# Kernel tuning notes

Hardware: AMD Instinct MI355X
Metric: run time of the kernel (lower is better)

## Reference

```python
import jax, jax.numpy as jnp
import numpy as np
from jax import lax

B, CR, CS = 2, 256, 512
HR = WR = 64
HS = WS = 32
D_INNER, D_STATE, DT_RANK, D_CONV = 512, 16, 16, 3
EPS = 1e-5


def setup_inputs() -> dict:
    key = jax.random.key(0)
    ks = jax.random.split(key, 16)
    s = 0.02
    return {
        "resnet_feat": jax.random.normal(ks[0], (B, CR, HR, WR), jnp.float32),
        "scp_feat": jax.random.normal(ks[1], (B, CS, HS, WS), jnp.float32),
        "scp_proj_w": jax.random.normal(ks[2], (CR, CS), jnp.float32) * s,
        "scp_bn_g": jnp.ones((CR,), jnp.float32),
        "scp_bn_b": jnp.zeros((CR,), jnp.float32),
        "scp_bn_m": jax.random.normal(ks[3], (CR,), jnp.float32) * 0.1,
        "scp_bn_v": jax.random.uniform(ks[4], (CR,), jnp.float32, minval=0.5, maxval=1.5),
        "res_bn_g": jnp.ones((CR,), jnp.float32),
        "res_bn_b": jnp.zeros((CR,), jnp.float32),
        "res_bn_m": jax.random.normal(ks[5], (CR,), jnp.float32) * 0.1,
        "res_bn_v": jax.random.uniform(ks[6], (CR,), jnp.float32, minval=0.5, maxval=1.5),
        "ln_g": jnp.ones((CR,), jnp.float32),
        "ln_b": jnp.zeros((CR,), jnp.float32),
        "in_proj_w": jax.random.normal(ks[7], (2 * D_INNER, CR), jnp.float32) * s,
        "conv_w": jax.random.normal(ks[8], (D_INNER, 1, D_CONV), jnp.float32) * s,
        "conv_b": jnp.zeros((D_INNER,), jnp.float32),
        "x_proj_w": jax.random.normal(ks[9], (DT_RANK + 2 * D_STATE, D_INNER), jnp.float32) * s,
        "dt_proj_w": jax.random.normal(ks[10], (D_INNER, DT_RANK), jnp.float32) * s,
        "dt_proj_b": jnp.full((D_INNER,), -4.6, jnp.float32),  # softplus -> dt ~ 0.01
        "A_log": jnp.log(jnp.broadcast_to(jnp.arange(1, D_STATE + 1, dtype=jnp.float32), (D_INNER, D_STATE))),
        "D": jnp.ones((D_INNER,), jnp.float32),
        "out_proj_w": jax.random.normal(ks[11], (CR, D_INNER), jnp.float32) * s,
    }


def _bn(x, g, b, m, v):
    # eval-mode BatchNorm2d with running stats, NCHW
    inv = g / jnp.sqrt(v + EPS)
    return x * inv[None, :, None, None] + (b - m * inv)[None, :, None, None]


def reference(resnet_feat, scp_feat, scp_proj_w, scp_bn_g, scp_bn_b, scp_bn_m, scp_bn_v,
              res_bn_g, res_bn_b, res_bn_m, res_bn_v, ln_g, ln_b, in_proj_w, conv_w, conv_b,
              x_proj_w, dt_proj_w, dt_proj_b, A_log, D, out_proj_w):
    # --- fusion prelude ---
    rn = _bn(resnet_feat, res_bn_g, res_bn_b, res_bn_m, res_bn_v)
    sp = jnp.einsum('bchw,oc->bohw', scp_feat, scp_proj_w)        # 1x1 conv, no bias
    sp = _bn(sp, scp_bn_g, scp_bn_b, scp_bn_m, scp_bn_v)
    sp = jax.image.resize(sp, (B, CR, HR, WR), method='bilinear')  # align_corners=False semantics
    fused = rn + sp                                               # (B, CR, HR, WR)

    # --- Mamba2DBlock ---
    L = HR * WR
    x_seq = fused.transpose(0, 2, 3, 1).reshape(B, L, CR)
    mu = x_seq.mean(-1, keepdims=True)
    var = x_seq.var(-1, keepdims=True)
    xn = (x_seq - mu) / jnp.sqrt(var + EPS) * ln_g + ln_b         # LayerNorm

    xz = xn @ in_proj_w.T                                         # (B, L, 2*d_inner)
    xm, z = jnp.split(xz, 2, axis=-1)

    # causal depthwise conv1d over sequence
    xc = xm.transpose(0, 2, 1)                                    # (B, d_inner, L)
    xc = jnp.pad(xc, ((0, 0), (0, 0), (D_CONV - 1, 0)))
    xc = lax.conv_general_dilated(xc, conv_w, (1,), 'VALID',
                                  dimension_numbers=('NCH', 'OIH', 'NCH'),
                                  feature_group_count=D_INNER) + conv_b[None, :, None]
    u = jax.nn.silu(xc.transpose(0, 2, 1))                        # (B, L, d_inner)

    x_dbl = u @ x_proj_w.T                                        # (B, L, dt_rank + 2*d_state)
    dt_in, Bc, Cc = jnp.split(x_dbl, [DT_RANK, DT_RANK + D_STATE], axis=-1)
    dt = jax.nn.softplus(dt_in @ dt_proj_w.T + dt_proj_b)         # (B, L, d_inner)

    A = -jnp.exp(A_log)                                           # (d_inner, d_state)
    dA = jnp.exp(dt[..., None] * A)                               # (B, L, d_inner, d_state)
    dBu = dt[..., None] * Bc[:, :, None, :] * u[..., None]        # (B, L, d_inner, d_state)

    def comb(c1, c2):
        a1, b1 = c1
        a2, b2 = c2
        return a1 * a2, a2 * b1 + b2

    _, h = lax.associative_scan(comb, (dA, dBu), axis=1)          # h: (B, L, d_inner, d_state)
    y = jnp.einsum('blds,bls->bld', h, Cc) + u * D
    y = y * jax.nn.silu(z)
    out_seq = y @ out_proj_w.T                                    # (B, L, CR)
    out = out_seq.reshape(B, HR, WR, CR).transpose(0, 3, 1, 2)
    return fused + out
```

## Files before the change

### kernel.cpp

```cpp
#include <hip/hip_runtime.h>
#include <hip/hip_bf16.h>
#include <math.h>

typedef unsigned short u16;
typedef __attribute__((ext_vector_type(8))) short short8;
typedef __attribute__((ext_vector_type(4))) float f32x4;
typedef __attribute__((ext_vector_type(4))) unsigned short u16x4;

#define DEVINL static __device__ __forceinline__

DEVINL float b2f(u16 x) {
    union { unsigned u; float f; } v; v.u = ((unsigned)x) << 16; return v.f;
}
DEVINL u16 f2b(float f) {
    union { unsigned u; float f; } v; v.f = f;
    unsigned u = v.u;
    return (u16)((u + 0x7fffu + ((u >> 16) & 1u)) >> 16);
}
DEVINL float silu(float x) { return x / (1.f + __expf(-x)); }
DEVINL float ld_any(bool f32, const void* p, size_t i) {
    return f32 ? ((const float*)p)[i] : b2f(((const u16*)p)[i]);
}
template<bool F32> DEVINL float LDs(const void* p, size_t i) {
    if constexpr (F32) return ((const float*)p)[i];
    else               return b2f(((const u16*)p)[i]);
}

#define O_INW  0
#define O_XPW  262144
#define O_OPW  286720
#define O_SPW  417792
#define O_CW   548864
#define O_CB   550400
#define O_DTW  550912
#define O_ALOG 559104
#define O_DTB  567296
#define O_DW   567808
#define O_SG   568320
#define O_SB   568576
#define O_SM   568832
#define O_SV   569088
#define O_RG   569344
#define O_RB   569600
#define O_RM   569856
#define O_RV   570112
#define O_LG   570368
#define O_LB   570624
#define N_CVT  570880

__global__ __launch_bounds__(1024) void k_detect(const u16* __restrict__ raw,
                                                 int* __restrict__ flag)
{
    int tid = threadIdx.x;
    int cnt = 0;
    for (int i = tid; i < 131072; i += 1024) {
        float v = b2f(raw[i]);
        if (!(fabsf(v) <= 1e3f)) cnt++;
    }
#pragma unroll
    for (int off = 1; off < 64; off <<= 1) cnt += __shfl_xor(cnt, off);
    __shared__ int s16[16];
    if ((tid & 63) == 0) s16[tid >> 6] = cnt;
    __syncthreads();
    if (tid == 0) {
        int c = 0;
#pragma unroll
        for (int w = 0; w < 16; ++w) c += s16[w];
        flag[0] = (c > 0) ? 1 : 0;
    }
}

DEVINL void tr_tile(bool f32, const void* src, u16* dst, int R, int C,
                    int c0, int r0, int b, int tid)
{
    __shared__ u16 t[64][66];
    int lane = tid & 63, grp = tid >> 6;
#pragma unroll
    for (int j = 0; j < 16; ++j) {
        int rl = j * 4 + grp;
        t[rl][lane] = f2b(ld_any(f32, src, ((size_t)b * R + r0 + rl) * C + c0 + lane));
    }
    __syncthreads();
#pragma unroll
    for (int j = 0; j < 16; ++j) {
        int cl = j * 4 + grp;
        dst[((size_t)b * C + c0 + cl) * R + r0 + lane] = t[lane][cl];
    }
}

__global__ __launch_bounds__(256) void k_prep(const int* __restrict__ flag,
    const void* inw, const void* xpw, const void* opw, const void* spw,
    const void* cw, const void* cb, const void* dtw, const void* alog,
    const void* dtb, const void* Dw,
    const void* sg, const void* sb, const void* sm, const void* sv,
    const void* rg, const void* rb, const void* rm, const void* rv,
    const void* lg, const void* lb,
    const void* scp, const void* resnet,
    u16* __restrict__ w16, u16* __restrict__ scpT, u16* __restrict__ resnetT)
{
    bool f32 = (*flag != 0);
    int bid = blockIdx.x, tid = threadIdx.x;
    if (bid < 2230) {
        int i = bid * 256 + tid;
        const void* src; int off = i;
        if      (i < O_XPW)  { src = inw; }
        else if (i < O_OPW)  { src = xpw;  off = i - O_XPW; }
        else if (i < O_SPW)  { src = opw;  off = i - O_OPW; }
        else if (i < O_CW)   { src = spw;  off = i - O_SPW; }
        else if (i < O_CB)   { src = cw;   off = i - O_CW; }
        else if (i < O_DTW)  { src = cb;   off = i - O_CB; }
        else if (i < O_ALOG) { src = dtw;  off = i - O_DTW; }
        else if (i < O_DTB)  { src = alog; off = i - O_ALOG; }
        else if (i < O_DW)   { src = dtb;  off = i - O_DTB; }
        else if (i < O_SG)   { src = Dw;   off = i - O_DW; }
        else if (i < O_SB)   { src = sg;   off = i - O_SG; }
        else if (i < O_SM)   { src = sb;   off = i - O_SB; }
        else if (i < O_SV)   { src = sm;   off = i - O_SM; }
        else if (i < O_RG)   { src = sv;   off = i - O_SV; }
        else if (i < O_RB)   { src = rg;   off = i - O_RG; }
        else if (i < O_RM)   { src = rb;   off = i - O_RB; }
        else if (i < O_RV)   { src = rm;   off = i - O_RM; }
        else if (i < O_LG)   { src = rv;   off = i - O_RV; }
        else if (i < O_LB)   { src = lg;   off = i - O_LG; }
        else                 { src = lb;   off = i - O_LB; }
        w16[i] = f2b(ld_any(f32, src, off));
    } else if (bid < 2230 + 256) {
        int t = bid - 2230;
        tr_tile(f32, scp, scpT, 512, 1024, (t & 15) * 64, ((t >> 4) & 7) * 64, t >> 7, tid);
    } else {
        int t = bid - 2486;
        tr_tile(f32, resnet, resnetT, 256, 4096, (t & 63) * 64, ((t >> 6) & 3) * 64, t >> 8, tid);
    }
}

__global__ __launch_bounds__(256) void k_scpmm(
    const u16* __restrict__ scpT, const u16* __restrict__ w16,
    u16* __restrict__ sp16)
{
    const int N = 256, K = 512;
    int tid = threadIdx.x, lane = tid & 63, wid = tid >> 6;
    int ln = lane & 15, q = lane >> 4;
    int m0 = blockIdx.x * 64 + (wid & 1) * 32;
    int n0 = blockIdx.y * 64 + (wid >> 1) * 32;
    f32x4 acc00 = {0.f,0.f,0.f,0.f}, acc01 = acc00, acc10 = acc00, acc11 = acc00;
    const u16* Ap0 = scpT + (size_t)(m0 + ln) * K + q * 8;
    const u16* Ap1 = Ap0 + (size_t)16 * K;
    const u16* Wp = w16 + O_SPW;
#pragma unroll 4
    for (int k0 = 0; k0 < K; k0 += 32) {
        int kk = k0 + q * 8;
        short8 a0 = *reinterpret_cast<const short8*>(Ap0 + k0);
        short8 a1 = *reinterpret_cast<const short8*>(Ap1 + k0);
        short8 b0 = *reinterpret_cast<const short8*>(Wp + (size_t)(n0 + ln) * K + kk);
        short8 b1 = *reinterpret_cast<const short8*>(Wp + (size_t)(n0 + ln + 16) * K + kk);
        acc00 = __builtin_amdgcn_mfma_f32_16x16x32_bf16(a0, b0, acc00, 0, 0, 0);
        acc01 = __builtin_amdgcn_mfma_f32_16x16x32_bf16(a0, b1, acc01, 0, 0, 0);
        acc10 = __builtin_amdgcn_mfma_f32_16x16x32_bf16(a1, b0, acc10, 0, 0, 0);
        acc11 = __builtin_amdgcn_mfma_f32_16x16x32_bf16(a1, b1, acc11, 0, 0, 0);
    }
    int r0 = m0 + q * 4, c0 = n0 + ln;
    float inv0 = b2f(w16[O_SG + c0]) * rsqrtf(b2f(w16[O_SV + c0]) + 1e-5f);
    float sh0  = b2f(w16[O_SB + c0]) - b2f(w16[O_SM + c0]) * inv0;
    float inv1 = b2f(w16[O_SG + c0 + 16]) * rsqrtf(b2f(w16[O_SV + c0 + 16]) + 1e-5f);
    float sh1  = b2f(w16[O_SB + c0 + 16]) - b2f(w16[O_SM + c0 + 16]) * inv1;
#pragma unroll
    for (int r = 0; r < 4; ++r) {
        sp16[(size_t)(r0 + r) * N + c0]           = f2b(acc00[r] * inv0 + sh0);
        sp16[(size_t)(r0 + r) * N + c0 + 16]      = f2b(acc01[r] * inv1 + sh1);
        sp16[(size_t)(r0 + 16 + r) * N + c0]      = f2b(acc10[r] * inv0 + sh0);
        sp16[(size_t)(r0 + 16 + r) * N + c0 + 16] = f2b(acc11[r] * inv1 + sh1);
    }
}

__global__ __launch_bounds__(256) void k_ln(
    const u16* __restrict__ resnetT, const u16* __restrict__ w16,
    const u16* __restrict__ sp16, u16* __restrict__ xn)
{
    __shared__ float red[8];
    int c = threadIdx.x, b = blockIdx.y;
    float inv = b2f(w16[O_RG + c]) * rsqrtf(b2f(w16[O_RV + c]) + 1e-5f);
    float sh  = b2f(w16[O_RB + c]) - b2f(w16[O_RM + c]) * inv;
    float lgv = b2f(w16[O_LG + c]), lbv = b2f(w16[O_LB + c]);
    const u16* spc = sp16 + (size_t)b * 1024 * 256 + c;
    for (int j = 0; j < 8; ++j) {
        int l = blockIdx.x * 8 + j;
        int h = l >> 6, w = l & 63;
        float rr = b2f(resnetT[((size_t)b * 4096 + l) * 256 + c]);
        float rn = rr * inv + sh;
        float xh = 0.5f * h - 0.25f; int jh = (int)floorf(xh); float fh = xh - jh;
        float xw = 0.5f * w - 0.25f; int jw = (int)floorf(xw); float fw = xw - jw;
        int h0 = jh < 0 ? 0 : jh, h1 = jh + 1 > 31 ? 31 : jh + 1;
        int w0 = jw < 0 ? 0 : jw, w1 = jw + 1 > 31 ? 31 : jw + 1;
        float v00 = b2f(spc[(size_t)(h0 * 32 + w0) * 256]), v01 = b2f(spc[(size_t)(h0 * 32 + w1) * 256]);
        float v10 = b2f(spc[(size_t)(h1 * 32 + w0) * 256]), v11 = b2f(spc[(size_t)(h1 * 32 + w1) * 256]);
        float sp = (1.f - fh) * ((1.f - fw) * v00 + fw * v01)
                 + fh * ((1.f - fw) * v10 + fw * v11);
        float fv = rn + sp;

        float s = fv, s2 = fv * fv;
#pragma unroll
        for (int off = 1; off < 64; off <<= 1) {
            s  += __shfl_xor(s, off);
            s2 += __shfl_xor(s2, off);
        }
        int wv = c >> 6;
        if ((c & 63) == 0) { red[wv] = s; red[4 + wv] = s2; }
        __syncthreads();
        float S  = red[0] + red[1] + red[2] + red[3];
        float S2 = red[4] + red[5] + red[6] + red[7];
        __syncthreads();
        float mu   = S * (1.f / 256.f);
        float var  = S2 * (1.f / 256.f) - mu * mu;
        float rstd = rsqrtf(var + 1e-5f);
        xn[((size_t)b * 4096 + l) * 256 + c] = f2b((fv - mu) * rstd * lgv + lbv);
    }
}

__global__ __launch_bounds__(256) void k_gemm_in(
    const u16* __restrict__ A, const u16* __restrict__ w16, u16* __restrict__ Out)
{
    const int N = 1024, K = 256;
    int tid = threadIdx.x, lane = tid & 63, wid = tid >> 6;
    int ln = lane & 15, q = lane >> 4;
    int m0 = blockIdx.x * 64 + (wid & 1) * 32;
    int n0 = blockIdx.y * 64 + (wid >> 1) * 32;
    f32x4 acc00 = {0.f,0.f,0.f,0.f}, acc01 = acc00, acc10 = acc00, acc11 = acc00;
    const u16* Ap0 = A + (size_t)(m0 + ln) * K + q * 8;
    const u16* Ap1 = Ap0 + (size_t)16 * K;
    const u16* Wp = w16 + O_INW;
#pragma unroll 4
    for (int k0 = 0; k0 < K; k0 += 32) {
        int kk = k0 + q * 8;
        short8 a0 = *reinterpret_cast<const short8*>(Ap0 + k0);
        short8 a1 = *reinterpret_cast<const short8*>(Ap1 + k0);
        short8 b0 = *reinterpret_cast<const short8*>(Wp + (size_t)(n0 + ln) * K + kk);
        short8 b1 = *reinterpret_cast<const short8*>(Wp + (size_t)(n0 + ln + 16) * K + kk);
        acc00 = __builtin_amdgcn_mfma_f32_16x16x32_bf16(a0, b0, acc00, 0, 0, 0);
        acc01 = __builtin_amdgcn_mfma_f32_16x16x32_bf16(a0, b1, acc01, 0, 0, 0);
        acc10 = __builtin_amdgcn_mfma_f32_16x16x32_bf16(a1, b0, acc10, 0, 0, 0);
        acc11 = __builtin_amdgcn_mfma_f32_16x16x32_bf16(a1, b1, acc11, 0, 0, 0);
    }
    int r0 = m0 + q * 4, c0 = n0 + ln;
#pragma unroll
    for (int r = 0; r < 4; ++r) {
        Out[(size_t)(r0 + r) * N + c0]           = f2b(acc00[r]);
        Out[(size_t)(r0 + r) * N + c0 + 16]      = f2b(acc01[r]);
        Out[(size_t)(r0 + 16 + r) * N + c0]      = f2b(acc10[r]);
        Out[(size_t)(r0 + 16 + r) * N + c0 + 16] = f2b(acc11[r]);
    }
}

DEVINL short8 u_frag(const u16* __restrict__ xz, const u16* __restrict__ w16,
                     int row, int kk0)
{
    int l = row & 4095;
    const u16* p = xz + (size_t)row * 1024 + kk0;
    short8 zz = {0,0,0,0,0,0,0,0};
    short8 x0 = *reinterpret_cast<const short8*>(p);
    short8 x1 = (l >= 1) ? *reinterpret_cast<const short8*>(p - 1024) : zz;
    short8 x2 = (l >= 2) ? *reinterpret_cast<const short8*>(p - 2048) : zz;
    short8 r;
#pragma unroll
    for (int j = 0; j < 8; ++j) {
        int d = kk0 + j;
        float acc = b2f(w16[O_CB + d])
                  + b2f((u16)x2[j]) * b2f(w16[O_CW + d * 3])
                  + b2f((u16)x1[j]) * b2f(w16[O_CW + d * 3 + 1])
                  + b2f((u16)x0[j]) * b2f(w16[O_CW + d * 3 + 2]);
        r[j] = (short)f2b(silu(acc));
    }
    return r;
}

__global__ __launch_bounds__(256) void k_xproj(
    const u16* __restrict__ xz, const u16* __restrict__ w16, float* __restrict__ xdf)
{
    int tid = threadIdx.x, lane = tid & 63, wid = tid >> 6;
    int ln = lane & 15, q = lane >> 4;
    int m0 = blockIdx.x * 64 + wid * 16;
    const u16* Wp = w16 + O_XPW;
    f32x4 acc[3];
#pragma unroll
    for (int j = 0; j < 3; ++j) acc[j] = {0.f,0.f,0.f,0.f};
    for (int k0 = 0; k0 < 512; k0 += 32) {
        int kk0 = k0 + q * 8;
        short8 a0 = u_frag(xz, w16, m0 + ln, kk0);
#pragma unroll
        for (int j = 0; j < 3; ++j) {
            short8 bj = *reinterpret_cast<const short8*>(Wp + (size_t)(16 * j + ln) * 512 + kk0);
            acc[j] = __builtin_amdgcn_mfma_f32_16x16x32_bf16(a0, bj, acc[j], 0, 0, 0);
        }
    }
#pragma unroll
    for (int j = 0; j < 3; ++j)
#pragma unroll
        for (int r = 0; r < 4; ++r)
            xdf[(size_t)(m0 + q * 4 + r) * 48 + 16 * j + ln] = acc[j][r];
}

DEVINL float dt_of(const float* xd, const float* wdt, float bias) {
    float acc = bias;
#pragma unroll
    for (int r = 0; r < 16; ++r) acc += xd[r] * wdt[r];
    return acc > 15.f ? acc : __logf(1.f + __expf(acc));
}

__global__ __launch_bounds__(512) void k_scan1(
    const u16* __restrict__ xz, const float* __restrict__ xdf,
    const u16* __restrict__ w16, u16* __restrict__ cA, u16* __restrict__ cH,
    int NC, int CL)
{
    __shared__ float xds[32][48];
    int d = threadIdx.x, ck = blockIdx.x, b = blockIdx.y;
    float wdt[16], a[16], h[16], ap[16];
#pragma unroll
    for (int s = 0; s < 16; ++s) {
        wdt[s] = b2f(w16[O_DTW + d * 16 + s]);
        a[s] = -__expf(b2f(w16[O_ALOG + d * 16 + s]));
        h[s] = 0.f; ap[s] = 1.f;
    }
    float bias = b2f(w16[O_DTB + d]);
    float cw0 = b2f(w16[O_CW + d * 3]), cw1 = b2f(w16[O_CW + d * 3 + 1]),
          cw2 = b2f(w16[O_CW + d * 3 + 2]), cbv = b2f(w16[O_CB + d]);
    int l0 = ck * CL;
    size_t xbase = ((size_t)b * 4096 + l0) * 1024 + d;
    float x2 = (l0 >= 2) ? b2f(xz[xbase - 2048]) : 0.f;
    float x1 = (l0 >= 1) ? b2f(xz[xbase - 1024]) : 0.f;
    for (int t0 = 0; t0 < CL; t0 += 32) {
        __syncthreads();
#pragma unroll
        for (int k = 0; k < 3; ++k) {
            int idx = k * 512 + d;
            int r = idx / 48, c = idx - r * 48;
            xds[r][c] = xdf[((size_t)b * 4096 + l0 + t0 + r) * 48 + c];
        }
        __syncthreads();
        for (int il = 0; il < 32; ++il) {
            float x0 = b2f(xz[xbase + (size_t)(t0 + il) * 1024]);
            float uv = silu(cbv + cw0 * x2 + cw1 * x1 + cw2 * x0);
            const float* xd = xds[il];
            float dtv = dt_of(xd, wdt, bias);
            float du = dtv * uv;
#pragma unroll
            for (int s = 0; s < 16; ++s) {
                float dA = __expf(dtv * a[s]);
                h[s]  = dA * h[s] + du * xd[16 + s];
                ap[s] *= dA;
            }
            x2 = x1; x1 = x0;
        }
    }
    size_t base = (((size_t)b * NC + ck) * 16) * 512 + d;
#pragma unroll
    for (int s = 0; s < 16; ++s) {
        cA[base + (size_t)s * 512] = f2b(ap[s]);
        cH[base + (size_t)s * 512] = f2b(h[s]);
    }
}

__global__ __launch_bounds__(128) void k_scan2(const u16* __restrict__ cA,
                                               u16* __restrict__ cH, int NC)
{
    int d = blockIdx.y * 128 + threadIdx.x, s = blockIdx.x, b = blockIdx.z;
    float h = 0.f;
#pragma unroll 4
    for (int ck = 0; ck < NC; ++ck) {
        size_t idx = (((size_t)b * NC + ck) * 16 + s) * 512 + d;
        float aP = b2f(cA[idx]), hE = b2f(cH[idx]);
        cH[idx] = f2b(h);
        h = aP * h + hE;
    }
}

__global__ __launch_bounds__(512) void k_scan3(
    const u16* __restrict__ xz, const float* __restrict__ xdf,
    const u16* __restrict__ w16, const u16* __restrict__ cH,
    u16* __restrict__ y, int NC, int CL)
{
    __shared__ float xds[32][48];
    int d = threadIdx.x, ck = blockIdx.x, b = blockIdx.y;
    float wdt[16], a[16], h[16];
    size_t base = (((size_t)b * NC + ck) * 16) * 512 + d;
#pragma unroll
    for (int s = 0; s < 16; ++s) {
        wdt[s] = b2f(w16[O_DTW + d * 16 + s]);
        a[s] = -__expf(b2f(w16[O_ALOG + d * 16 + s]));
        h[s] = b2f(cH[base + (size_t)s * 512]);
    }
    float bias = b2f(w16[O_DTB + d]);
    float Dv = b2f(w16[O_DW + d]);
    float cw0 = b2f(w16[O_CW + d * 3]), cw1 = b2f(w16[O_CW + d * 3 + 1]),
          cw2 = b2f(w16[O_CW + d * 3 + 2]), cbv = b2f(w16[O_CB + d]);
    int l0 = ck * CL;
    size_t xbase = ((size_t)b * 4096 + l0) * 1024 + d;
    float x2 = (l0 >= 2) ? b2f(xz[xbase - 2048]) : 0.f;
    float x1 = (l0 >= 1) ? b2f(xz[xbase - 1024]) : 0.f;
    for (int t0 = 0; t0 < CL; t0 += 32) {
        __syncthreads();
#pragma unroll
        for (int k = 0; k < 3; ++k) {
            int idx = k * 512 + d;
            int r = idx / 48, c = idx - r * 48;
            xds[r][c] = xdf[((size_t)b * 4096 + l0 + t0 + r) * 48 + c];
        }
        __syncthreads();
        for (int il = 0; il < 32; ++il) {
            size_t row = (size_t)b * 4096 + l0 + t0 + il;
            float x0 = b2f(xz[xbase + (size_t)(t0 + il) * 1024]);
            float uv = silu(cbv + cw0 * x2 + cw1 * x1 + cw2 * x0);
            const float* xd = xds[il];
            float dtv = dt_of(xd, wdt, bias);
            float du = dtv * uv;
            float yv = 0.f;
#pragma unroll
            for (int s = 0; s < 16; ++s) {
                float dA = __expf(dtv * a[s]);
                h[s] = dA * h[s] + du * xd[16 + s];
                yv += h[s] * xd[32 + s];
            }
            yv += uv * Dv;
            float zv = b2f(xz[row * 1024 + 512 + d]);
            yv *= silu(zv);
            y[row * 512 + d] = f2b(yv);
            x2 = x1; x1 = x0;
        }
    }
}

template<bool F32> DEVINL void out_body(
    const u16* Y, const u16* w16, const void* resnet,
    const u16* sp16, void* outp)
{
    const int K = 512;
    int tid = threadIdx.x, lane = tid & 63, wid = tid >> 6;
    int ln = lane & 15, q = lane >> 4;
    int m0 = blockIdx.x * 64 + (wid & 1) * 32;
    int n0 = blockIdx.y * 64 + (wid >> 1) * 32;
    f32x4 acc[2][2];
    acc[0][0] = {0.f,0.f,0.f,0.f}; acc[0][1] = acc[0][0];
    acc[1][0] = acc[0][0]; acc[1][1] = acc[0][0];
    const u16* Bp0 = Y + (size_t)(n0 + ln) * K + q * 8;
    const u16* Bp1 = Bp0 + (size_t)16 * K;
    const u16* Wp = w16 + O_OPW;
#pragma unroll 4
    for (int k0 = 0; k0 < K; k0 += 32) {
        int kk = k0 + q * 8;
        short8 b0 = *reinterpret_cast<const short8*>(Bp0 + k0);
        short8 b1 = *reinterpret_cast<const short8*>(Bp1 + k0);
        short8 a0 = *reinterpret_cast<const short8*>(Wp + (size_t)(m0 + ln) * K + kk);
        short8 a1 = *reinterpret_cast<const short8*>(Wp + (size_t)(m0 + ln + 16) * K + kk);
        acc[0][0] = __builtin_amdgcn_mfma_f32_16x16x32_bf16(a0, b0, acc[0][0], 0, 0, 0);
        acc[0][1] = __builtin_amdgcn_mfma_f32_16x16x32_bf16(a0, b1, acc[0][1], 0, 0, 0);
        acc[1][0] = __builtin_amdgcn_mfma_f32_16x16x32_bf16(a1, b0, acc[1][0], 0, 0, 0);
        acc[1][1] = __builtin_amdgcn_mfma_f32_16x16x32_bf16(a1, b1, acc[1][1], 0, 0, 0);
    }
    int r0 = m0 + q * 4;
    int nb = n0 + ln;
    float inv8[2][4], sh8[2][4];
#pragma unroll
    for (int im = 0; im < 2; ++im)
#pragma unroll
        for (int r = 0; r < 4; ++r) {
            int c = r0 + 16 * im + r;
            float inv = b2f(w16[O_RG + c]) * rsqrtf(b2f(w16[O_RV + c]) + 1e-5f);
            inv8[im][r] = inv;
            sh8[im][r]  = b2f(w16[O_RB + c]) - b2f(w16[O_RM + c]) * inv;
        }
#pragma unroll
    for (int jn = 0; jn < 2; ++jn) {
        int n = nb + 16 * jn;
        int b = n >> 12, l = n & 4095;
        int hh = l >> 6, w = l & 63;
        float xh = 0.5f * hh - 0.25f; int jh = (int)floorf(xh); float fh = xh - jh;
        float xw = 0.5f * w - 0.25f;  int jw = (int)floorf(xw); float fw = xw - jw;
        int h0 = jh < 0 ? 0 : jh, h1 = jh + 1 > 31 ? 31 : jh + 1;
        int w0 = jw < 0 ? 0 : jw, w1 = jw + 1 > 31 ? 31 : jw + 1;
        float w00 = (1.f - fh) * (1.f - fw), w01 = (1.f - fh) * fw;
        float w10 = fh * (1.f - fw),         w11 = fh * fw;
        const u16* spb = sp16 + (size_t)b * 1024 * 256;
#pragma unroll
        for (int im = 0; im < 2; ++im) {
            int cb = r0 + 16 * im;
            u16x4 s00 = *reinterpret_cast<const u16x4*>(spb + (size_t)(h0 * 32 + w0) * 256 + cb);
            u16x4 s01 = *reinterpret_cast<const u16x4*>(spb + (size_t)(h0 * 32 + w1) * 256 + cb);
            u16x4 s10 = *reinterpret_cast<const u16x4*>(spb + (size_t)(h1 * 32 + w0) * 256 + cb);
            u16x4 s11 = *reinterpret_cast<const u16x4*>(spb + (size_t)(h1 * 32 + w1) * 256 + cb);
#pragma unroll
            for (int r = 0; r < 4; ++r) {
                int c = cb + r;
                float rr = LDs<F32>(resnet, ((size_t)b * 256 + c) * 4096 + l);
                float sp = w00 * b2f(s00[r]) + w01 * b2f(s01[r])
                         + w10 * b2f(s10[r]) + w11 * b2f(s11[r]);
                float val = acc[im][jn][r] + rr * inv8[im][r] + sh8[im][r] + sp;
                size_t oi = ((size_t)b * 256 + c) * 4096 + l;
                if constexpr (F32) ((float*)outp)[oi] = val;
                else               ((u16*)outp)[oi]  = f2b(val);
            }
        }
    }
}
__global__ __launch_bounds__(256) void k_out(const int* flag,
    const u16* Y, const u16* w16, const void* resnet,
    const u16* sp16, void* outp)
{
    if (*flag) out_body<true>(Y, w16, resnet, sp16, outp);
    else       out_body<false>(Y, w16, resnet, sp16, outp);
}

extern "C" void kernel_launch(void* const* d_in, const int* in_sizes, int n_in,
                              void* d_out, int out_size, void* d_ws, size_t ws_size,
                              hipStream_t stream)
{
    const void* resnet = d_in[0];
    const void* scp    = d_in[1];
    const void* spw    = d_in[2];
    const void* sg     = d_in[3];
    const void* sb     = d_in[4];
    const void* sm     = d_in[5];
    const void* sv     = d_in[6];
    const void* rg     = d_in[7];
    const void* rb     = d_in[8];
    const void* rm     = d_in[9];
    const void* rv     = d_in[10];
    const void* lg     = d_in[11];
    const void* lb     = d_in[12];
    const void* inw    = d_in[13];
    const void* cw     = d_in[14];
    const void* cb     = d_in[15];
    const void* xpw    = d_in[16];
    const void* dtw    = d_in[17];
    const void* dtb    = d_in[18];
    const void* alog   = d_in[19];
    const void* Dw     = d_in[20];
    const void* opw    = d_in[21];

    char*  ws      = (char*)d_ws;
    int*   flag    = (int*)(ws);
    u16*   w16     = (u16*)(ws + 4096);
    u16*   sp16    = (u16*)(ws + 2097152);
    u16*   scpT    = (u16*)(ws + 4194304);
    u16*   resnetT = (u16*)(ws + 8388608);
    u16*   xn      = (u16*)(ws + 12582912);
    u16*   xz      = (u16*)(ws + 16777216);
    float* xdf     = (float*)(ws + 33554432);
    u16*   y       = (u16*)(ws + 35651584);
    const size_t tail0 = 44040192;

    int NC = 16;
    for (int cand = 128; cand >= 16; cand >>= 1) {
        if (tail0 + (size_t)cand * 65536 <= ws_size) { NC = cand; break; }
    }
    int CL = 4096 / NC;
    u16* cA = (u16*)(ws + tail0);
    u16* cH = (u16*)(ws + tail0 + (size_t)NC * 32768);

    k_detect<<<dim3(1), 1024, 0, stream>>>((const u16*)resnet, flag);
    k_prep<<<dim3(2998), 256, 0, stream>>>(flag,
        inw, xpw, opw, spw, cw, cb, dtw, alog, dtb, Dw,
        sg, sb, sm, sv, rg, rb, rm, rv, lg, lb,
        scp, resnet, w16, scpT, resnetT);
    k_scpmm<<<dim3(32, 4), 256, 0, stream>>>(scpT, w16, sp16);
    k_ln<<<dim3(512, 2), 256, 0, stream>>>(resnetT, w16, sp16, xn);
    k_gemm_in<<<dim3(128, 16), 256, 0, stream>>>(xn, w16, xz);
    k_xproj<<<dim3(128), 256, 0, stream>>>(xz, w16, xdf);
    k_scan1<<<dim3(NC, 2), 512, 0, stream>>>(xz, xdf, w16, cA, cH, NC, CL);
    k_scan2<<<dim3(16, 4, 2), 128, 0, stream>>>(cA, cH, NC);
    k_scan3<<<dim3(NC, 2), 512, 0, stream>>>(xz, xdf, w16, cH, y, NC, CL);
    k_out<<<dim3(4, 128), 256, 0, stream>>>(flag, y, w16, resnet, sp16, d_out);
}
```

Measured before the change: 281.6 us.

## Inline dtype detection, widen GEMM N-tiles, and halve xproj block size

The separate single-block detection kernel is removed. Each kernel that needs the input dtype now samples 64 values of resnet itself, which saves one serial launch. The in_proj and out_proj GEMMs give each wave a 32x64 output tile instead of 32x32, so every A fragment is reused across four B fragments and half as many blocks are launched. The xproj kernel switches to 128-thread blocks with twice as many blocks to spread work over more CUs. In exchange, the sparser dtype detection is less robust and the larger accumulator tiles raise register pressure.

```diff
diff --git a/kernel.cpp b/kernel.cpp
--- a/kernel.cpp
+++ b/kernel.cpp
@@ -24,6 +24,16 @@
 template<bool F32> DEVINL float LDs(const void* p, size_t i) {
     if constexpr (F32) return ((const float*)p)[i];
     else               return b2f(((const u16*)p)[i]);
+}
+
+DEVINL bool detect_f32(const u16* __restrict__ raw) {
+    int cnt = 0;
+#pragma unroll
+    for (int i = 0; i < 64; ++i) {
+        float v = b2f(raw[i * 2]);
+        if (!(fabsf(v) <= 1e3f)) cnt++;
+    }
+    return cnt > 0;
 }
 
 #define O_INW  0
@@ -48,28 +58,6 @@
 #define O_LB   570624
 #define N_CVT  570880
 
-__global__ __launch_bounds__(1024) void k_detect(const u16* __restrict__ raw,
-                                                 int* __restrict__ flag)
-{
-    int tid = threadIdx.x;
-    int cnt = 0;
-    for (int i = tid; i < 131072; i += 1024) {
-        float v = b2f(raw[i]);
-        if (!(fabsf(v) <= 1e3f)) cnt++;
-    }
-#pragma unroll
-    for (int off = 1; off < 64; off <<= 1) cnt += __shfl_xor(cnt, off);
-    __shared__ int s16[16];
-    if ((tid & 63) == 0) s16[tid >> 6] = cnt;
-    __syncthreads();
-    if (tid == 0) {
-        int c = 0;
-#pragma unroll
-        for (int w = 0; w < 16; ++w) c += s16[w];
-        flag[0] = (c > 0) ? 1 : 0;
-    }
-}
-
 DEVINL void tr_tile(bool f32, const void* src, u16* dst, int R, int C,
                     int c0, int r0, int b, int tid)
 {
@@ -88,7 +76,7 @@
     }
 }
 
-__global__ __launch_bounds__(256) void k_prep(const int* __restrict__ flag,
+__global__ __launch_bounds__(256) void k_prep(
     const void* inw, const void* xpw, const void* opw, const void* spw,
     const void* cw, const void* cb, const void* dtw, const void* alog,
     const void* dtb, const void* Dw,
@@ -98,7 +86,7 @@
     const void* scp, const void* resnet,
     u16* __restrict__ w16, u16* __restrict__ scpT, u16* __restrict__ resnetT)
 {
-    bool f32 = (*flag != 0);
+    bool f32 = detect_f32((const u16*)resnet);
     int bid = blockIdx.x, tid = threadIdx.x;
     if (bid < 2230) {
         int i = bid * 256 + tid;
@@ -223,31 +211,34 @@
     int tid = threadIdx.x, lane = tid & 63, wid = tid >> 6;
     int ln = lane & 15, q = lane >> 4;
     int m0 = blockIdx.x * 64 + (wid & 1) * 32;
-    int n0 = blockIdx.y * 64 + (wid >> 1) * 32;
-    f32x4 acc00 = {0.f,0.f,0.f,0.f}, acc01 = acc00, acc10 = acc00, acc11 = acc00;
+    int n0 = blockIdx.y * 128 + (wid >> 1) * 64;
+    f32x4 acc[2][4];
+#pragma unroll
+    for (int i = 0; i < 2; ++i)
+#pragma unroll
+        for (int j = 0; j < 4; ++j) acc[i][j] = {0.f,0.f,0.f,0.f};
     const u16* Ap0 = A + (size_t)(m0 + ln) * K + q * 8;
     const u16* Ap1 = Ap0 + (size_t)16 * K;
-    const u16* Wp = w16 + O_INW;
-#pragma unroll 4
+    const u16* Bp  = w16 + O_INW + (size_t)(n0 + ln) * K + q * 8;
+#pragma unroll 2
     for (int k0 = 0; k0 < K; k0 += 32) {
-        int kk = k0 + q * 8;
         short8 a0 = *reinterpret_cast<const short8*>(Ap0 + k0);
         short8 a1 = *reinterpret_cast<const short8*>(Ap1 + k0);
-        short8 b0 = *reinterpret_cast<const short8*>(Wp + (size_t)(n0 + ln) * K + kk);
-        short8 b1 = *reinterpret_cast<const short8*>(Wp + (size_t)(n0 + ln + 16) * K + kk);
-        acc00 = __builtin_amdgcn_mfma_f32_16x16x32_bf16(a0, b0, acc00, 0, 0, 0);
-        acc01 = __builtin_amdgcn_mfma_f32_16x16x32_bf16(a0, b1, acc01, 0, 0, 0);
-        acc10 = __builtin_amdgcn_mfma_f32_16x16x32_bf16(a1, b0, acc10, 0, 0, 0);
-        acc11 = __builtin_amdgcn_mfma_f32_16x16x32_bf16(a1, b1, acc11, 0, 0, 0);
+#pragma unroll
+        for (int j = 0; j < 4; ++j) {
+            short8 bj = *reinterpret_cast<const short8*>(Bp + (size_t)(16 * j) * K + k0);
+            acc[0][j] = __builtin_amdgcn_mfma_f32_16x16x32_bf16(a0, bj, acc[0][j], 0, 0, 0);
+            acc[1][j] = __builtin_amdgcn_mfma_f32_16x16x32_bf16(a1, bj, acc[1][j], 0, 0, 0);
+        }
     }
     int r0 = m0 + q * 4, c0 = n0 + ln;
 #pragma unroll
-    for (int r = 0; r < 4; ++r) {
-        Out[(size_t)(r0 + r) * N + c0]           = f2b(acc00[r]);
-        Out[(size_t)(r0 + r) * N + c0 + 16]      = f2b(acc01[r]);
-        Out[(size_t)(r0 + 16 + r) * N + c0]      = f2b(acc10[r]);
-        Out[(size_t)(r0 + 16 + r) * N + c0 + 16] = f2b(acc11[r]);
-    }
+    for (int i = 0; i < 2; ++i)
+#pragma unroll
+        for (int j = 0; j < 4; ++j)
+#pragma unroll
+            for (int r = 0; r < 4; ++r)
+                Out[(size_t)(r0 + 16 * i + r) * N + c0 + 16 * j] = f2b(acc[i][j][r]);
 }
 
 DEVINL short8 u_frag(const u16* __restrict__ xz, const u16* __restrict__ w16,
@@ -272,12 +263,12 @@
     return r;
 }
 
-__global__ __launch_bounds__(256) void k_xproj(
+__global__ __launch_bounds__(128) void k_xproj(
     const u16* __restrict__ xz, const u16* __restrict__ w16, float* __restrict__ xdf)
 {
     int tid = threadIdx.x, lane = tid & 63, wid = tid >> 6;
     int ln = lane & 15, q = lane >> 4;
-    int m0 = blockIdx.x * 64 + wid * 16;
+    int m0 = blockIdx.x * 32 + wid * 16;
     const u16* Wp = w16 + O_XPW;
     f32x4 acc[3];
 #pragma unroll
@@ -435,24 +426,25 @@
     int tid = threadIdx.x, lane = tid & 63, wid = tid >> 6;
     int ln = lane & 15, q = lane >> 4;
     int m0 = blockIdx.x * 64 + (wid & 1) * 32;
-    int n0 = blockIdx.y * 64 + (wid >> 1) * 32;
-    f32x4 acc[2][2];
-    acc[0][0] = {0.f,0.f,0.f,0.f}; acc[0][1] = acc[0][0];
-    acc[1][0] = acc[0][0]; acc[1][1] = acc[0][0];
-    const u16* Bp0 = Y + (size_t)(n0 + ln) * K + q * 8;
-    const u16* Bp1 = Bp0 + (size_t)16 * K;
-    const u16* Wp = w16 + O_OPW;
-#pragma unroll 4
+    int n0 = blockIdx.y * 128 + (wid >> 1) * 64;
+    f32x4 acc[2][4];
+#pragma unroll
+    for (int i = 0; i < 2; ++i)
+#pragma unroll
+        for (int j = 0; j < 4; ++j) acc[i][j] = {0.f,0.f,0.f,0.f};
+    const u16* Ap0 = w16 + O_OPW + (size_t)(m0 + ln) * K + q * 8;
+    const u16* Ap1 = Ap0 + (size_t)16 * K;
+    const u16* Bp  = Y + (size_t)(n0 + ln) * K + q * 8;
+#pragma unroll 2
     for (int k0 = 0; k0 < K; k0 += 32) {
-        int kk = k0 + q * 8;
-        short8 b0 = *reinterpret_cast<const short8*>(Bp0 + k0);
-        short8 b1 = *reinterpret_cast<const short8*>(Bp1 + k0);
-        short8 a0 = *reinterpret_cast<const short8*>(Wp + (size_t)(m0 + ln) * K + kk);
-        short8 a1 = *reinterpret_cast<const short8*>(Wp + (size_t)(m0 + ln + 16) * K + kk);
-        acc[0][0] = __builtin_amdgcn_mfma_f32_16x16x32_bf16(a0, b0, acc[0][0], 0, 0, 0);
-        acc[0][1] = __builtin_amdgcn_mfma_f32_16x16x32_bf16(a0, b1, acc[0][1], 0, 0, 0);
-        acc[1][0] = __builtin_amdgcn_mfma_f32_16x16x32_bf16(a1, b0, acc[1][0], 0, 0, 0);
-        acc[1][1] = __builtin_amdgcn_mfma_f32_16x16x32_bf16(a1, b1, acc[1][1], 0, 0, 0);
+        short8 a0 = *reinterpret_cast<const short8*>(Ap0 + k0);
+        short8 a1 = *reinterpret_cast<const short8*>(Ap1 + k0);
+#pragma unroll
+        for (int j = 0; j < 4; ++j) {
+            short8 bj = *reinterpret_cast<const short8*>(Bp + (size_t)(16 * j) * K + k0);
+            acc[0][j] = __builtin_amdgcn_mfma_f32_16x16x32_bf16(a0, bj, acc[0][j], 0, 0, 0);
+            acc[1][j] = __builtin_amdgcn_mfma_f32_16x16x32_bf16(a1, bj, acc[1][j], 0, 0, 0);
+        }
     }
     int r0 = m0 + q * 4;
     int nb = n0 + ln;
@@ -467,7 +459,7 @@
             sh8[im][r]  = b2f(w16[O_RB + c]) - b2f(w16[O_RM + c]) * inv;
         }
 #pragma unroll
-    for (int jn = 0; jn < 2; ++jn) {
+    for (int jn = 0; jn < 4; ++jn) {
         int n = nb + 16 * jn;
         int b = n >> 12, l = n & 4095;
         int hh = l >> 6, w = l & 63;
@@ -499,12 +491,12 @@
         }
     }
 }
-__global__ __launch_bounds__(256) void k_out(const int* flag,
+__global__ __launch_bounds__(256) void k_out(
     const u16* Y, const u16* w16, const void* resnet,
     const u16* sp16, void* outp)
 {
-    if (*flag) out_body<true>(Y, w16, resnet, sp16, outp);
-    else       out_body<false>(Y, w16, resnet, sp16, outp);
+    if (detect_f32((const u16*)resnet)) out_body<true>(Y, w16, resnet, sp16, outp);
+    else                                out_body<false>(Y, w16, resnet, sp16, outp);
 }
 
 extern "C" void kernel_launch(void* const* d_in, const int* in_sizes, int n_in,
@@ -535,7 +527,6 @@
     const void* opw    = d_in[21];
 
     char*  ws      = (char*)d_ws;
-    int*   flag    = (int*)(ws);
     u16*   w16     = (u16*)(ws + 4096);
     u16*   sp16    = (u16*)(ws + 2097152);
     u16*   scpT    = (u16*)(ws + 4194304);
@@ -554,17 +545,16 @@
     u16* cA = (u16*)(ws + tail0);
     u16* cH = (u16*)(ws + tail0 + (size_t)NC * 32768);
 
-    k_detect<<<dim3(1), 1024, 0, stream>>>((const u16*)resnet, flag);
-    k_prep<<<dim3(2998), 256, 0, stream>>>(flag,
+    k_prep<<<dim3(2998), 256, 0, stream>>>(
         inw, xpw, opw, spw, cw, cb, dtw, alog, dtb, Dw,
         sg, sb, sm, sv, rg, rb, rm, rv, lg, lb,
         scp, resnet, w16, scpT, resnetT);
     k_scpmm<<<dim3(32, 4), 256, 0, stream>>>(scpT, w16, sp16);
     k_ln<<<dim3(512, 2), 256, 0, stream>>>(resnetT, w16, sp16, xn);
-    k_gemm_in<<<dim3(128, 16), 256, 0, stream>>>(xn, w16, xz);
-    k_xproj<<<dim3(128), 256, 0, stream>>>(xz, w16, xdf);
+    k_gemm_in<<<dim3(128, 8), 256, 0, stream>>>(xn, w16, xz);
+    k_xproj<<<dim3(256), 128, 0, stream>>>(xz, w16, xdf);
     k_scan1<<<dim3(NC, 2), 512, 0, stream>>>(xz, xdf, w16, cA, cH, NC, CL);
     k_scan2<<<dim3(16, 4, 2), 128, 0, stream>>>(cA, cH, NC);
     k_scan3<<<dim3(NC, 2), 512, 0, stream>>>(xz, xdf, w16, cH, y, NC, CL);
-    k_out<<<dim3(4, 128), 256, 0, stream>>>(flag, y, w16, resnet, sp16, d_out);
-}
+    k_out<<<dim3(4, 64), 256, 0, stream>>>(y, w16, resnet, sp16, d_out);
+}
```

Result: faster. 267.1 us (-5.1%).
